# Kernel tuning notes

Measured on AMD Instinct MI355X. Metric: run time of the kernel, lower is better.

The kernel has to match this reference:

```python
import jax, jax.numpy as jnp
import numpy as np

H = 12          # heads in the ViT blocks
D = 768         # model dim (hard-coded in the module)
DFF = 3072      # mlp hidden = 4*D
ADIM = 64       # adapter bottleneck dim
L = 32          # num_latents
EPS = 1e-6      # timm ViT LayerNorm eps


def _ln(x, g, b):
    m = jnp.mean(x, axis=-1, keepdims=True)
    v = jnp.var(x, axis=-1, keepdims=True)
    return (x - m) * jax.lax.rsqrt(v + EPS) * g + b


def _quick_gelu(x):
    return x * jax.nn.sigmoid(1.702 * x)


def _sh_attn(q, k, v):
    # single-head attention used by fusion(); scale = C**-0.5 with C = full dim
    C = q.shape[-1]
    a = jax.nn.softmax(jnp.einsum('bnc,bmc->bnm', q, k) * (C ** -0.5), axis=-1)
    return jnp.einsum('bnm,bmc->bnc', a, v)


def _mhsa(x, qkv_w, qkv_b, proj_w, proj_b):
    B, N, C = x.shape
    Dh = C // H
    qkv = (x @ qkv_w.T + qkv_b).reshape(B, N, 3, H, Dh).transpose(2, 0, 3, 1, 4)
    q, k, v = qkv[0], qkv[1], qkv[2]                       # [B,H,N,Dh]
    a = jax.nn.softmax(jnp.einsum('bhnd,bhmd->bhnm', q, k) * (Dh ** -0.5), axis=-1)
    o = jnp.einsum('bhnm,bhmd->bhnd', a, v).transpose(0, 2, 1, 3).reshape(B, N, C)
    return o @ proj_w.T + proj_b


def _stream(t, ln1_g, ln1_b, qkv_w, qkv_b, proj_w, proj_b,
            ln2_g, ln2_b, fc1_w, fc1_b, fc2_w, fc2_b,
            down_w, down_b, up_w, up_b, scale):
    t = t + _mhsa(_ln(t, ln1_g, ln1_b), qkv_w, qkv_b, proj_w, proj_b)
    h = _ln(t, ln2_g, ln2_b)
    mlp = jax.nn.gelu(h @ fc1_w.T + fc1_b, approximate=False) @ fc2_w.T + fc2_b
    adapter = (_quick_gelu(h @ down_w.T + down_b) @ up_w.T + up_b) * scale
    return t + mlp + adapter


def setup_inputs() -> dict:
    key = jax.random.key(0)
    ks = iter(jax.random.split(key, 64))
    f32 = jnp.float32
    def rn(shape, std=0.02):
        return (jax.random.normal(next(ks), shape, dtype=f32) * std)
    inp = {
        'x': jax.random.normal(next(ks), (16, 512, 768), dtype=f32),
        'y': jax.random.normal(next(ks), (16, 196, 768), dtype=f32),
        'latents': rn((1, L, D)),
        'scale_a': jnp.full((1,), 0.5, f32),
        'scale_v': jnp.full((1,), 0.5, f32),
    }
    for p in ('spec', 'rgb'):
        inp.update({
            f'{p}_ln1_g': jnp.ones((D,), f32), f'{p}_ln1_b': jnp.zeros((D,), f32),
            f'{p}_qkv_w': rn((3 * D, D)), f'{p}_qkv_b': jnp.zeros((3 * D,), f32),
            f'{p}_proj_w': rn((D, D)), f'{p}_proj_b': jnp.zeros((D,), f32),
            f'{p}_ln2_g': jnp.ones((D,), f32), f'{p}_ln2_b': jnp.zeros((D,), f32),
            f'{p}_fc1_w': rn((DFF, D)), f'{p}_fc1_b': jnp.zeros((DFF,), f32),
            f'{p}_fc2_w': rn((D, DFF)), f'{p}_fc2_b': jnp.zeros((D,), f32),
            f'{p}_down_w': rn((ADIM, D)), f'{p}_down_b': jnp.zeros((ADIM,), f32),
            f'{p}_up_w': rn((D, ADIM)), f'{p}_up_b': jnp.zeros((D,), f32),
            f'{p}_scale': jnp.ones((1,), f32),
        })
    return inp


def reference(x, y, latents, scale_a, scale_v,
              spec_ln1_g, spec_ln1_b, spec_qkv_w, spec_qkv_b, spec_proj_w, spec_proj_b,
              spec_ln2_g, spec_ln2_b, spec_fc1_w, spec_fc1_b, spec_fc2_w, spec_fc2_b,
              spec_down_w, spec_down_b, spec_up_w, spec_up_b, spec_scale,
              rgb_ln1_g, rgb_ln1_b, rgb_qkv_w, rgb_qkv_b, rgb_proj_w, rgb_proj_b,
              rgb_ln2_g, rgb_ln2_b, rgb_fc1_w, rgb_fc1_b, rgb_fc2_w, rgb_fc2_b,
              rgb_down_w, rgb_down_b, rgb_up_w, rgb_up_b, rgb_scale):
    B = x.shape[0]
    # --- fusion via latent bottleneck (single-head attention) ---
    concat_ = jnp.concatenate((x, y), axis=1)                 # [B, Na+Nv, D]
    lat = jnp.broadcast_to(latents, (B, L, D))
    fused = _sh_attn(lat, concat_, concat_)                   # [B, L, D]
    x = x + scale_a * _sh_attn(x, fused, fused)
    y = y + scale_v * _sh_attn(y, fused, fused)
    # --- per-stream transformer block + adapter (dropout = eval/identity) ---
    x = _stream(x, spec_ln1_g, spec_ln1_b, spec_qkv_w, spec_qkv_b, spec_proj_w, spec_proj_b,
                spec_ln2_g, spec_ln2_b, spec_fc1_w, spec_fc1_b, spec_fc2_w, spec_fc2_b,
                spec_down_w, spec_down_b, spec_up_w, spec_up_b, spec_scale)
    y = _stream(y, rgb_ln1_g, rgb_ln1_b, rgb_qkv_w, rgb_qkv_b, rgb_proj_w, rgb_proj_b,
                rgb_ln2_g, rgb_ln2_b, rgb_fc1_w, rgb_fc1_b, rgb_fc2_w, rgb_fc2_b,
                rgb_down_w, rgb_down_b, rgb_up_w, rgb_up_b, rgb_scale)
    return (x, y)
```

## Files before the change

### kernel.cpp

```cpp
#include <hip/hip_runtime.h>
#include <hip/hip_bf16.h>


#define H_HEADS 12
#define DMODEL 768
#define DFF 3072
#define ADIM 64
#define NLAT 32
#define BATCH 16
#define NA 512
#define NV 196
#define NTOT 708
#define MCAT (BATCH * NTOT)
#define MTOT (BATCH * (NA + NV))

typedef __hip_bfloat16 bf16;
using bf16x8 = __attribute__((ext_vector_type(8))) short;
using f32x4  = __attribute__((ext_vector_type(4))) float;

static __device__ __forceinline__ float bf2f(bf16 v) { return __bfloat162float(v); }
static __device__ __forceinline__ float bflo(unsigned u) { return __uint_as_float(u << 16); }
static __device__ __forceinline__ float ld1(const float* p) { return *p; }
static __device__ __forceinline__ float ld1(const bf16* p) { return bf2f(*p); }
static __device__ __forceinline__ unsigned short f2bf_bits(float v) {
    unsigned u = __float_as_uint(v);
    return (unsigned short)((u + 0x7fffu + ((u >> 16) & 1u)) >> 16);
}

#define GLD_LDS16(gp, lp) __builtin_amdgcn_global_load_lds( \
    (const __attribute__((address_space(1))) void*)(gp), \
    (__attribute__((address_space(3))) void*)(lp), 16, 0, 0)

static inline int pad8(int v) { return (v + 7) & ~7; }

__global__ void detect_dtype_kernel(const unsigned short* __restrict__ x, int* __restrict__ flag)
{
    if (threadIdx.x == 0 && blockIdx.x == 0) {
        int big = 0;
        for (int i = 0; i < 2048; i++) {
            unsigned e = (x[i] >> 7) & 0xFF;
            if (e >= 0x90) big++;
        }
        flag[0] = (big > 16) ? 1 : 0;
        flag[1] = 0;
    }
}

template<typename TIn>
static __device__ __forceinline__ void pack_body(
    const TIn* __restrict__ x, const TIn* __restrict__ y, const TIn* __restrict__ lat,
    bf16* __restrict__ Cc, bf16* __restrict__ Lb)
{
    const int r = blockIdx.x, tid = threadIdx.x;
    const TIn* src;
    bf16* dst;
    if (r < MCAT) {
        const int b = r / NTOT, n = r - b * NTOT;
        src = (n < NA) ? x + ((size_t)(b * NA + n)) * DMODEL
                       : y + ((size_t)(b * NV + (n - NA))) * DMODEL;
        dst = Cc + (size_t)r * DMODEL;
    } else {
        src = lat + (size_t)(r - MCAT) * DMODEL;
        dst = Lb + (size_t)(r - MCAT) * DMODEL;
    }
    dst[tid]       = __float2bfloat16(ld1(src + tid));
    dst[tid + 256] = __float2bfloat16(ld1(src + tid + 256));
    dst[tid + 512] = __float2bfloat16(ld1(src + tid + 512));
}

__global__ __launch_bounds__(256)
void pack_concat_kernel(const int* __restrict__ flag, const void* x, const void* y,
                        const void* lat, bf16* __restrict__ Cc, bf16* __restrict__ Lb)
{
    if (flag[0]) pack_body<float>((const float*)x, (const float*)y, (const float*)lat, Cc, Lb);
    else         pack_body<bf16>((const bf16*)x, (const bf16*)y, (const bf16*)lat, Cc, Lb);
}

__global__ __launch_bounds__(64)
void fusion_softmax_kernel(const float* __restrict__ scores, float* __restrict__ P)
{
    const int b = blockIdx.x >> 5, l = blockIdx.x & 31, lane = threadIdx.x;
    const float* sp = scores + (size_t)b * NTOT * NLAT + l;
    float v[12];
    float mx = -1e30f;
    #pragma unroll
    for (int i = 0; i < 12; i++) {
        const int n = lane + i * 64;
        v[i] = (n < NTOT) ? sp[(size_t)n * NLAT] * 0.03608439182435161f : -1e30f;
        mx = fmaxf(mx, v[i]);
    }
    #pragma unroll
    for (int off = 32; off; off >>= 1) mx = fmaxf(mx, __shfl_xor(mx, off));
    float den = 0.f;
    #pragma unroll
    for (int i = 0; i < 12; i++) { v[i] = __expf(v[i] - mx); den += v[i]; }
    #pragma unroll
    for (int off = 32; off; off >>= 1) den += __shfl_xor(den, off);
    const float inv = 1.0f / den;
    float* op = P + ((size_t)b * NLAT + l) * 768;
    #pragma unroll
    for (int i = 0; i < 12; i++) {
        const int n = lane + i * 64;
        op[n] = (n < NTOT) ? v[i] * inv : 0.f;
    }
}

__global__ __launch_bounds__(256)
void fusion_wsum_kernel(const bf16* __restrict__ Cc, const float* __restrict__ P,
                        bf16* __restrict__ fused)
{
    const int b = blockIdx.y, d0 = blockIdx.x * 128;
    const int tid = threadIdx.x;
    const int lg = tid >> 5, dg = tid & 31;
    const int l0 = lg * 4;

    __shared__ float Ct[64][132];
    __shared__ float Ps[32][68];

    float acc[4][4] = {};

    for (int nc = 0; nc < 12; nc++) {
        const int n0 = nc * 64;
        __syncthreads();
        #pragma unroll
        for (int it = 0; it < 8; it++) {
            const int idx = it * 1024 + tid * 4;
            const int r = idx >> 7, c = idx & 127;
            const int gn = n0 + r;
            float4 v = make_float4(0.f, 0.f, 0.f, 0.f);
            if (gn < NTOT) {
                const ushort4 u = *(const ushort4*)(Cc + ((size_t)(b * NTOT + gn)) * DMODEL + d0 + c);
                v = make_float4(bflo(u.x), bflo(u.y), bflo(u.z), bflo(u.w));
            }
            Ct[r][c] = v.x; Ct[r][c + 1] = v.y; Ct[r][c + 2] = v.z; Ct[r][c + 3] = v.w;
        }
        {
            const int l = tid >> 3, off = (tid & 7) * 8;
            const float* pp = P + ((size_t)b * NLAT + l) * 768 + n0 + off;
            const float4 p0 = *(const float4*)pp;
            const float4 p1 = *(const float4*)(pp + 4);
            Ps[l][off] = p0.x; Ps[l][off + 1] = p0.y; Ps[l][off + 2] = p0.z; Ps[l][off + 3] = p0.w;
            Ps[l][off + 4] = p1.x; Ps[l][off + 5] = p1.y; Ps[l][off + 6] = p1.z; Ps[l][off + 7] = p1.w;
        }
        __syncthreads();

        for (int n = 0; n < 64; n++) {
            const float4 v = *(const float4*)&Ct[n][dg * 4];
            #pragma unroll
            for (int i = 0; i < 4; i++) {
                const float p = Ps[l0 + i][n];
                acc[i][0] += p * v.x; acc[i][1] += p * v.y;
                acc[i][2] += p * v.z; acc[i][3] += p * v.w;
            }
        }
    }

    #pragma unroll
    for (int i = 0; i < 4; i++) {
        bf16* op = fused + ((size_t)b * NLAT + l0 + i) * DMODEL + d0 + dg * 4;
        #pragma unroll
        for (int j = 0; j < 4; j++) op[j] = __float2bfloat16(acc[i][j]);
    }
}

template<typename TIn>
static __device__ __forceinline__ void attend_fused_body(
    const TIn* __restrict__ t, const bf16* __restrict__ fused,
    const TIn* __restrict__ scale_p, const TIn* __restrict__ lng, const TIn* __restrict__ lnb,
    bf16* __restrict__ out, bf16* __restrict__ hout, int Npb)
{
    const int tid = threadIdx.x;
    const int gid = blockIdx.x;
    const int b = gid / Npb;
    const TIn* row = t + (size_t)gid * DMODEL;
    const bf16* fb = fused + (size_t)b * NLAT * DMODEL;

    __shared__ float q[DMODEL];
    __shared__ float p[NLAT];
    __shared__ float rs[4], rq[4];

    for (int d = tid; d < DMODEL; d += 256) q[d] = ld1(row + d);
    __syncthreads();

    const int g = tid >> 3, li = tid & 7;
    float s = 0.f;
    const bf16* fr = fb + (size_t)g * DMODEL;
    for (int d = li; d < DMODEL; d += 8) s += q[d] * bf2f(fr[d]);
    s += __shfl_xor(s, 1); s += __shfl_xor(s, 2); s += __shfl_xor(s, 4);
    if (li == 0) p[g] = s * 0.03608439182435161f;
    __syncthreads();

    float mx = -1e30f;
    #pragma unroll
    for (int l = 0; l < NLAT; l++) mx = fmaxf(mx, p[l]);
    float w[NLAT];
    float den = 0.f;
    #pragma unroll
    for (int l = 0; l < NLAT; l++) { w[l] = __expf(p[l] - mx); den += w[l]; }
    const float sA = ld1(scale_p) / den;

    float a0 = 0.f, a1 = 0.f, a2 = 0.f;
    #pragma unroll
    for (int l = 0; l < NLAT; l++) {
        const bf16* fv = fb + (size_t)l * DMODEL;
        a0 += w[l] * bf2f(fv[tid]);
        a1 += w[l] * bf2f(fv[tid + 256]);
        a2 += w[l] * bf2f(fv[tid + 512]);
    }
    const float t0v = q[tid] + sA * a0;
    const float t1v = q[tid + 256] + sA * a1;
    const float t2v = q[tid + 512] + sA * a2;
    bf16* o = out + (size_t)gid * DMODEL;
    o[tid]       = __float2bfloat16(t0v);
    o[tid + 256] = __float2bfloat16(t1v);
    o[tid + 512] = __float2bfloat16(t2v);

    if (hout) {
        float ss = t0v + t1v + t2v;
        float sq = t0v * t0v + t1v * t1v + t2v * t2v;
        #pragma unroll
        for (int off = 32; off; off >>= 1) { ss += __shfl_xor(ss, off); sq += __shfl_xor(sq, off); }
        if ((tid & 63) == 0) { rs[tid >> 6] = ss; rq[tid >> 6] = sq; }
        __syncthreads();
        ss = rs[0] + rs[1] + rs[2] + rs[3];
        sq = rq[0] + rq[1] + rq[2] + rq[3];
        const float mean = ss * (1.0f / DMODEL);
        const float var = sq * (1.0f / DMODEL) - mean * mean;
        const float r = rsqrtf(var + 1e-6f);
        bf16* ho = hout + (size_t)gid * DMODEL;
        ho[tid]       = __float2bfloat16((t0v - mean) * r * ld1(lng + tid)       + ld1(lnb + tid));
        ho[tid + 256] = __float2bfloat16((t1v - mean) * r * ld1(lng + tid + 256) + ld1(lnb + tid + 256));
        ho[tid + 512] = __float2bfloat16((t2v - mean) * r * ld1(lng + tid + 512) + ld1(lnb + tid + 512));
    }
}

__global__ __launch_bounds__(256)
void attend_fused_kernel(const int* __restrict__ flag, const void* t, const bf16* __restrict__ fused,
                         const void* scale_p, const void* lng, const void* lnb,
                         bf16* __restrict__ out, bf16* __restrict__ hout, int Npb)
{
    if (flag[0]) attend_fused_body<float>((const float*)t, fused, (const float*)scale_p,
                                          (const float*)lng, (const float*)lnb, out, hout, Npb);
    else         attend_fused_body<bf16>((const bf16*)t, fused, (const bf16*)scale_p,
                                         (const bf16*)lng, (const bf16*)lnb, out, hout, Npb);
}

template<typename TW>
static __device__ __forceinline__ void ln_body(
    const bf16* __restrict__ in, const TW* __restrict__ g,
    const TW* __restrict__ bta, bf16* __restrict__ out)
{
    const int tid = threadIdx.x;
    const bf16* p = in + (size_t)blockIdx.x * DMODEL;
    const float v0 = bf2f(p[tid]), v1 = bf2f(p[tid + 256]), v2 = bf2f(p[tid + 512]);
    float s = v0 + v1 + v2;
    float sq = v0 * v0 + v1 * v1 + v2 * v2;
    #pragma unroll
    for (int off = 32; off; off >>= 1) { s += __shfl_xor(s, off); sq += __shfl_xor(sq, off); }
    __shared__ float rs[4], rq[4];
    if ((tid & 63) == 0) { rs[tid >> 6] = s; rq[tid >> 6] = sq; }
    __syncthreads();
    s = rs[0] + rs[1] + rs[2] + rs[3];
    sq = rq[0] + rq[1] + rq[2] + rq[3];
    const float mean = s * (1.0f / DMODEL);
    const float var = sq * (1.0f / DMODEL) - mean * mean;
    const float r = rsqrtf(var + 1e-6f);
    bf16* o = out + (size_t)blockIdx.x * DMODEL;
    o[tid]       = __float2bfloat16((v0 - mean) * r * ld1(g + tid)       + ld1(bta + tid));
    o[tid + 256] = __float2bfloat16((v1 - mean) * r * ld1(g + tid + 256) + ld1(bta + tid + 256));
    o[tid + 512] = __float2bfloat16((v2 - mean) * r * ld1(g + tid + 512) + ld1(bta + tid + 512));
}

__global__ __launch_bounds__(256)
void ln_kernel(const int* __restrict__ flag, const bf16* __restrict__ in,
               const void* g0, const void* b0, const void* g1, const void* b1,
               bf16* __restrict__ out, int split)
{
    const bool isY = (int)blockIdx.x >= split;
    const void* g = isY ? g1 : g0;
    const void* b = isY ? b1 : b0;
    if (flag[0]) ln_body<float>(in, (const float*)g, (const float*)b, out);
    else         ln_body<bf16>(in, (const bf16*)g, (const bf16*)b, out);
}

__global__ __launch_bounds__(256)
void flash_attn_kernel(const bf16* __restrict__ qkv, bf16* __restrict__ o, int Npb)
{
    const int tid = threadIdx.x;
    const int wv = tid >> 6, lane = tid & 63;
    const int l15 = lane & 15, q4 = lane >> 4;
    const int h = blockIdx.x % H_HEADS, bb = blockIdx.x / H_HEADS;
    const int qt = blockIdx.y;
    const int nkv = (Npb + 63) >> 6;
    const size_t tokbase = (size_t)bb * Npb;

    __shared__ __align__(16) short Ks[64 * 64];
    __shared__ __align__(16) short Vt[64 * 64];
    __shared__ __align__(16) short Ps[4][16 * 64];

    const int qr = min(qt * 64 + wv * 16 + l15, Npb - 1);
    const bf16* qp = qkv + (tokbase + qr) * 2304 + h * 64;
    const bf16x8 qf0 = *(const bf16x8*)(const void*)(qp + q4 * 8);
    const bf16x8 qf1 = *(const bf16x8*)(const void*)(qp + 32 + q4 * 8);

    f32x4 Oa[4] = {};
    float mrow[4], lrow[4];
    #pragma unroll
    for (int i = 0; i < 4; i++) { mrow[i] = -1e30f; lrow[i] = 0.f; }

    for (int kv = 0; kv < nkv; kv++) {
        const int kv0 = kv * 64;
        __syncthreads();
        #pragma unroll
        for (int inst = 0; inst < 2; inst++) {
            const int s = inst * 256 + tid;
            const int row = s >> 3, pos = s & 7;
            const int c = pos ^ (row & 7);
            const int krc = min(kv0 + row, Npb - 1);
            GLD_LDS16(qkv + (tokbase + krc) * 2304 + DMODEL + h * 64 + c * 8, &Ks[s * 8]);
        }
        {
            const int r = tid >> 2;
            const int f0 = (tid & 3) * 16;
            const int krc = min(kv0 + r, Npb - 1);
            const short* vp = (const short*)(qkv + (tokbase + krc) * 2304 + 2 * DMODEL + h * 64 + f0);
            short vb[16];
            *(uint4*)&vb[0] = *(const uint4*)vp;
            *(uint4*)&vb[8] = *(const uint4*)(vp + 8);
            const int chunk = r >> 3, r7 = r & 7;
            #pragma unroll
            for (int j = 0; j < 16; j++) {
                const int feat = f0 + j;
                Vt[feat * 64 + (chunk ^ (feat & 7)) * 8 + r7] = vb[j];
            }
        }
        __syncthreads();

        f32x4 s4[4] = {};
        #pragma unroll
        for (int kk = 0; kk < 2; kk++) {
            const bf16x8 qf = kk ? qf1 : qf0;
            const int c = kk * 4 + q4;
            #pragma unroll
            for (int g = 0; g < 4; g++) {
                const int r = g * 16 + l15;
                const bf16x8 kf = *(const bf16x8*)(const void*)&Ks[r * 64 + (c ^ (r & 7)) * 8];
                s4[g] = __builtin_amdgcn_mfma_f32_16x16x32_bf16(qf, kf, s4[g], 0, 0, 0);
            }
        }
        float tmax[4];
        #pragma unroll
        for (int i = 0; i < 4; i++) tmax[i] = -1e30f;
        #pragma unroll
        for (int g = 0; g < 4; g++) {
            const bool valid = (kv0 + g * 16 + l15) < Npb;
            #pragma unroll
            for (int i = 0; i < 4; i++) {
                const float v = s4[g][i] * 0.125f;
                s4[g][i] = valid ? v : -1e30f;
                tmax[i] = fmaxf(tmax[i], s4[g][i]);
            }
        }
        #pragma unroll
        for (int off = 1; off < 16; off <<= 1)
            #pragma unroll
            for (int i = 0; i < 4; i++) tmax[i] = fmaxf(tmax[i], __shfl_xor(tmax[i], off));
        float alpha[4], rsum[4];
        #pragma unroll
        for (int i = 0; i < 4; i++) {
            const float mn = fmaxf(mrow[i], tmax[i]);
            alpha[i] = __expf(mrow[i] - mn);
            mrow[i] = mn;
            rsum[i] = 0.f;
        }
        #pragma unroll
        for (int g = 0; g < 4; g++) {
            const int cc = g * 16 + l15;
            const int chunk = cc >> 3;
            #pragma unroll
            for (int i = 0; i < 4; i++) {
                const int r = q4 * 4 + i;
                const float p = __expf(s4[g][i] - mrow[i]);
                rsum[i] += p;
                Ps[wv][r * 64 + (chunk ^ (r & 7)) * 8 + (cc & 7)] = (short)f2bf_bits(p);
            }
        }
        #pragma unroll
        for (int off = 1; off < 16; off <<= 1)
            #pragma unroll
            for (int i = 0; i < 4; i++) rsum[i] += __shfl_xor(rsum[i], off);
        #pragma unroll
        for (int i = 0; i < 4; i++) lrow[i] = lrow[i] * alpha[i] + rsum[i];
        #pragma unroll
        for (int g = 0; g < 4; g++)
            #pragma unroll
            for (int i = 0; i < 4; i++) Oa[g][i] *= alpha[i];

        #pragma unroll
        for (int kk = 0; kk < 2; kk++) {
            const int c = kk * 4 + q4;
            const bf16x8 pf = *(const bf16x8*)(const void*)&Ps[wv][l15 * 64 + (c ^ (l15 & 7)) * 8];
            #pragma unroll
            for (int g = 0; g < 4; g++) {
                const int feat = g * 16 + l15;
                const bf16x8 vf = *(const bf16x8*)(const void*)&Vt[feat * 64 + (c ^ (feat & 7)) * 8];
                Oa[g] = __builtin_amdgcn_mfma_f32_16x16x32_bf16(pf, vf, Oa[g], 0, 0, 0);
            }
        }
    }

    float inv[4];
    #pragma unroll
    for (int i = 0; i < 4; i++) inv[i] = 1.0f / lrow[i];
    #pragma unroll
    for (int g = 0; g < 4; g++) {
        const int colo = h * 64 + g * 16 + l15;
        #pragma unroll
        for (int i = 0; i < 4; i++) {
            const int rowg = qt * 64 + wv * 16 + q4 * 4 + i;
            if (rowg < Npb)
                o[(tokbase + rowg) * DMODEL + colo] = __float2bfloat16(Oa[g][i] * inv[i]);
        }
    }
}

template<int TM, int ACT, bool RES, bool SCALE, bool FD, typename TW>
static __device__ __forceinline__ void gemm_body(
    const bf16* __restrict__ A, const TW* __restrict__ W, const TW* __restrict__ Wd,
    const TW* __restrict__ bias, const TW* __restrict__ biasd,
    const bf16* __restrict__ resid, const TW* __restrict__ scale_p,
    void* __restrict__ C, bf16* __restrict__ Cd,
    bool cf32, int row_off, int M, int N, int K,
    short* As, short* Bs, float* Ep)
{
    const int tid = threadIdx.x;
    const int lane = tid & 63;
    const int wv = tid >> 6;
    const int l15 = lane & 15, q4 = lane >> 4;
    const int m0 = blockIdx.x * TM, n0 = blockIdx.y * 128;
    const int N1 = FD ? N - ADIM : N;
    constexpr int NF = (TM == 128) ? 4 : 2;
    const int wm = (TM == 128) ? (wv & 1) * 64 : 0;
    const int wn = (TM == 128) ? (wv >> 1) * 64 : wv * 32;

    f32x4 acc[4][NF] = {};

    for (int k0 = 0; k0 < K; k0 += 64) {
        __syncthreads();
        constexpr int AIT = TM * 8 / 256;
        #pragma unroll
        for (int it = 0; it < AIT; it++) {
            const int i = it * 256 + tid;
            const int row = i >> 3, pos = i & 7;
            const int c = pos ^ (row & 7);
            const int ra = min(m0 + row, M - 1);
            GLD_LDS16(A + (size_t)ra * K + k0 + c * 8, &As[i * 8]);
        }
        #pragma unroll
        for (int it = 0; it < 4; it++) {
            const int i = it * 256 + tid;
            const int row = i >> 3, pos = i & 7;
            const int c = pos ^ (row & 7);
            const int rb = min(n0 + row, N - 1);
            const TW* wp = (FD && rb >= N1) ? Wd + (size_t)(rb - N1) * K : W + (size_t)rb * K;
            if constexpr (sizeof(TW) == 2) {
                GLD_LDS16(wp + k0 + c * 8, &Bs[i * 8]);
            } else {
                const float* fp = (const float*)wp + k0 + c * 8;
                const float4 w0 = *(const float4*)fp;
                const float4 w1 = *(const float4*)(fp + 4);
                unsigned short hb[8];
                hb[0] = f2bf_bits(w0.x); hb[1] = f2bf_bits(w0.y);
                hb[2] = f2bf_bits(w0.z); hb[3] = f2bf_bits(w0.w);
                hb[4] = f2bf_bits(w1.x); hb[5] = f2bf_bits(w1.y);
                hb[6] = f2bf_bits(w1.z); hb[7] = f2bf_bits(w1.w);
                *(uint4*)&Bs[i * 8] = *(const uint4*)hb;
            }
        }
        __syncthreads();

        #pragma unroll
        for (int kk = 0; kk < 2; kk++) {
            bf16x8 af[4], bfr[NF];
            #pragma unroll
            for (int f = 0; f < 4; f++) {
                const int r = wm + f * 16 + l15;
                af[f] = *(const bf16x8*)(const void*)&As[(r * 8 + ((kk * 4 + q4) ^ (r & 7))) * 8];
            }
            #pragma unroll
            for (int g = 0; g < NF; g++) {
                const int rn = wn + g * 16 + l15;
                bfr[g] = *(const bf16x8*)(const void*)&Bs[(rn * 8 + ((kk * 4 + q4) ^ (rn & 7))) * 8];
            }
            #pragma unroll
            for (int f = 0; f < 4; f++)
                #pragma unroll
                for (int g = 0; g < NF; g++)
                    acc[f][g] = __builtin_amdgcn_mfma_f32_16x16x32_bf16(af[f], bfr[g], acc[f][g], 0, 0, 0);
        }
    }
    __syncthreads();

    const float sc = SCALE ? ld1(scale_p) : 1.0f;
    constexpr int NPASS = (TM == 128) ? 2 : 1;
    #pragma unroll
    for (int pass = 0; pass < NPASS; pass++) {
        if (wm == pass * 64) {
            #pragma unroll
            for (int g = 0; g < NF; g++) {
                const int col = wn + g * 16 + l15;
                const int colg = n0 + col;
                const bool isdown = FD && (colg >= N1);
                const float bv = bias ? (isdown ? ld1(biasd + (colg - N1)) : ld1(bias + colg)) : 0.f;
                #pragma unroll
                for (int f = 0; f < 4; f++) {
                    #pragma unroll
                    for (int i = 0; i < 4; i++) {
                        const int row = f * 16 + q4 * 4 + i;
                        float v = acc[f][g][i] + bv;
                        if (FD) {
                            if (isdown) v = v / (1.0f + __expf(-1.702f * v));
                            else v = 0.5f * v * (1.0f + erff(v * 0.70710678118654752f));
                        } else if (ACT == 1) v = 0.5f * v * (1.0f + erff(v * 0.70710678118654752f));
                        else if (ACT == 2) v = v / (1.0f + __expf(-1.702f * v));
                        if (SCALE) v *= sc;
                        const int c = col >> 2;
                        Ep[row * 128 + (((c ^ (row & 31))) << 2) + (col & 3)] = v;
                    }
                }
            }
        }
        __syncthreads();
        #pragma unroll
        for (int it = 0; it < 8; it++) {
            const int cid = it * 256 + tid;
            const int row = cid >> 5, c = cid & 31;
            const int rowg = m0 + pass * 64 + row;
            const int colg = n0 + c * 4;
            if (rowg < M && colg < N) {
                f32x4 v = *(const f32x4*)&Ep[row * 128 + (((c ^ (row & 31))) << 2)];
                if (FD && colg >= N1) {
                    ushort4 u;
                    u.x = f2bf_bits(v[0]); u.y = f2bf_bits(v[1]);
                    u.z = f2bf_bits(v[2]); u.w = f2bf_bits(v[3]);
                    *(ushort4*)(Cd + (size_t)rowg * ADIM + (colg - N1)) = u;
                } else {
                    if (RES) {
                        const ushort4 r4 = *(const ushort4*)(resid + (size_t)rowg * N + colg);
                        v[0] += bflo(r4.x); v[1] += bflo(r4.y);
                        v[2] += bflo(r4.z); v[3] += bflo(r4.w);
                    }
                    if (cf32) {
                        *(f32x4*)((float*)C + (size_t)(rowg + row_off) * N + colg) = v;
                    } else {
                        ushort4 u;
                        u.x = f2bf_bits(v[0]); u.y = f2bf_bits(v[1]);
                        u.z = f2bf_bits(v[2]); u.w = f2bf_bits(v[3]);
                        *(ushort4*)((bf16*)C + (size_t)(rowg + row_off) * (FD ? N1 : N) + colg) = u;
                    }
                }
            }
        }
        if (pass + 1 < NPASS) __syncthreads();
    }
}

template<int TM, int ACT, bool RES, bool SCALE, bool FD>
__global__ __launch_bounds__(256)
void mfma_gemm_kernel(const int* __restrict__ flag, const bf16* __restrict__ A,
                      const void* W0, const void* W1, const void* Wd0, const void* Wd1,
                      const void* b0, const void* b1, const void* bd0, const void* bd1,
                      const bf16* __restrict__ resid, const void* sp0, const void* sp1,
                      void* __restrict__ C, bf16* __restrict__ Cd,
                      int out_mode, int row_off, int M, int N, int K, int split)
{
    __shared__ __align__(16) char SMEM[32768];
    if ((int)blockIdx.x * TM >= M) return;
    const bool isY = ((int)blockIdx.x * TM) >= split;
    const void* W = isY ? W1 : W0;
    const void* Wd = isY ? Wd1 : Wd0;
    const void* bb = isY ? b1 : b0;
    const void* bd = isY ? bd1 : bd0;
    const void* sp = isY ? sp1 : sp0;
    short* As = (short*)SMEM;
    short* Bs = As + TM * 64;
    float* Ep = (float*)SMEM;
    const bool cf32 = (out_mode == 2) || (out_mode == 1 && flag[0] != 0);
    if (flag[0])
        gemm_body<TM, ACT, RES, SCALE, FD, float>(A, (const float*)W, (const float*)Wd,
            (const float*)bb, (const float*)bd, resid, (const float*)sp, C, Cd,
            cf32, row_off, M, N, K, As, Bs, Ep);
    else
        gemm_body<TM, ACT, RES, SCALE, FD, bf16>(A, (const bf16*)W, (const bf16*)Wd,
            (const bf16*)bb, (const bf16*)bd, resid, (const bf16*)sp, C, Cd,
            cf32, row_off, M, N, K, As, Bs, Ep);
}

struct SW {
    const void *ln1_g, *ln1_b, *qkv_w, *qkv_b, *proj_w, *proj_b,
               *ln2_g, *ln2_b, *fc1_w, *fc1_b, *fc2_w, *fc2_b,
               *down_w, *down_b, *up_w, *up_b, *scale;
};

static void stream_seq(const int* flag, bf16* t0, bf16* h, bf16* big, bf16* ah,
                       int M, int split, const SW& a, const SW& b,
                       void* outC, int row_off,
                       int npb0, int rows0, int npb1, int rows1, hipStream_t s)
{
    const dim3 gq(pad8((M + 127) / 128), 18);
    const dim3 gf(pad8((M + 127) / 128), 25);
    const dim3 g7(pad8((M + 63) / 64), 6);

    mfma_gemm_kernel<128, 0, false, false, false><<<gq, 256, 0, s>>>(flag, h,
        a.qkv_w, b.qkv_w, nullptr, nullptr, a.qkv_b, b.qkv_b, nullptr, nullptr,
        nullptr, nullptr, nullptr, big, nullptr, 0, 0, M, 2304, DMODEL, split);
    flash_attn_kernel<<<dim3((rows0 / npb0) * H_HEADS, (npb0 + 63) / 64), 256, 0, s>>>(big, h, npb0);
    if (rows1)
        flash_attn_kernel<<<dim3((rows1 / npb1) * H_HEADS, (npb1 + 63) / 64), 256, 0, s>>>(
            big + (size_t)rows0 * 2304, h + (size_t)rows0 * DMODEL, npb1);
    mfma_gemm_kernel<64, 0, true, false, false><<<g7, 256, 0, s>>>(flag, h,
        a.proj_w, b.proj_w, nullptr, nullptr, a.proj_b, b.proj_b, nullptr, nullptr,
        t0, nullptr, nullptr, t0, nullptr, 0, 0, M, DMODEL, DMODEL, split);
    ln_kernel<<<M, 256, 0, s>>>(flag, t0, a.ln2_g, a.ln2_b, b.ln2_g, b.ln2_b, h, split);
    mfma_gemm_kernel<128, 1, false, false, true><<<gf, 256, 0, s>>>(flag, h,
        a.fc1_w, b.fc1_w, a.down_w, b.down_w, a.fc1_b, b.fc1_b, a.down_b, b.down_b,
        nullptr, nullptr, nullptr, big, ah, 0, 0, M, DFF + ADIM, DMODEL, split);
    mfma_gemm_kernel<64, 0, true, false, false><<<g7, 256, 0, s>>>(flag, big,
        a.fc2_w, b.fc2_w, nullptr, nullptr, a.fc2_b, b.fc2_b, nullptr, nullptr,
        t0, nullptr, nullptr, t0, nullptr, 0, 0, M, DMODEL, DFF, split);
    mfma_gemm_kernel<64, 0, true, true, false><<<g7, 256, 0, s>>>(flag, ah,
        a.up_w, b.up_w, nullptr, nullptr, a.up_b, b.up_b, nullptr, nullptr,
        t0, a.scale, b.scale, outC, nullptr, 1, row_off, M, DMODEL, ADIM, split);
}

extern "C" void kernel_launch(void* const* d_in, const int* in_sizes, int n_in,
                              void* d_out, int out_size, void* d_ws, size_t ws_size,
                              hipStream_t stream)
{
    SW sw, rw;
    auto fill = [&](SW& s, int base) {
        s.ln1_g = d_in[base + 0];  s.ln1_b = d_in[base + 1];
        s.qkv_w = d_in[base + 2];  s.qkv_b = d_in[base + 3];
        s.proj_w = d_in[base + 4]; s.proj_b = d_in[base + 5];
        s.ln2_g = d_in[base + 6];  s.ln2_b = d_in[base + 7];
        s.fc1_w = d_in[base + 8];  s.fc1_b = d_in[base + 9];
        s.fc2_w = d_in[base + 10]; s.fc2_b = d_in[base + 11];
        s.down_w = d_in[base + 12]; s.down_b = d_in[base + 13];
        s.up_w = d_in[base + 14];  s.up_b = d_in[base + 15];
        s.scale = d_in[base + 16];
    };
    fill(sw, 5);
    fill(rw, 22);

    const int Mx = BATCH * NA;
    const int My = BATCH * NV;
    const int NOSPLIT = 1 << 30;

    const size_t szA = 256 + ((size_t)MTOT * DMODEL * 2 + (size_t)BATCH * NLAT * DMODEL
                     + (size_t)MTOT * DFF + (size_t)MTOT * ADIM) * 2;
    const size_t szB = 256 + ((size_t)Mx * DMODEL * 2 + (size_t)My * DMODEL
                     + (size_t)BATCH * NLAT * DMODEL + (size_t)Mx * DFF + (size_t)Mx * ADIM) * 2;

    int* flag = (int*)d_ws;
    detect_dtype_kernel<<<1, 64, 0, stream>>>((const unsigned short*)d_in[0], flag);

    if (ws_size >= szA) {
        char* base = (char*)d_ws + 256;
        bf16* t0 = (bf16*)base;      base += (size_t)MTOT * DMODEL * 2;
        bf16* fused = (bf16*)base;   base += (size_t)BATCH * NLAT * DMODEL * 2;
        bf16* h = (bf16*)base;       base += (size_t)MTOT * DMODEL * 2;
        bf16* big = (bf16*)base;     base += (size_t)MTOT * DFF * 2;
        bf16* ah = (bf16*)base;

        bf16* Cc = h;
        bf16* Lb = ah;
        float* scores = (float*)big;
        float* P = (float*)((char*)big + 2 * 1024 * 1024);

        pack_concat_kernel<<<MCAT + NLAT, 256, 0, stream>>>(flag, d_in[0], d_in[1], d_in[2], Cc, Lb);
        mfma_gemm_kernel<128, 0, false, false, false><<<dim3(pad8((MCAT + 127) / 128), 1), 256, 0, stream>>>(
            flag + 1, Cc, Lb, Lb, nullptr, nullptr, nullptr, nullptr, nullptr, nullptr,
            nullptr, nullptr, nullptr, scores, nullptr, 2, 0, MCAT, NLAT, DMODEL, NOSPLIT);
        fusion_softmax_kernel<<<BATCH * NLAT, 64, 0, stream>>>(scores, P);
        fusion_wsum_kernel<<<dim3(DMODEL / 128, BATCH), 256, 0, stream>>>(Cc, P, fused);

        attend_fused_kernel<<<BATCH * NA, 256, 0, stream>>>(
            flag, d_in[0], fused, d_in[3], sw.ln1_g, sw.ln1_b, t0, h, NA);
        attend_fused_kernel<<<BATCH * NV, 256, 0, stream>>>(
            flag, d_in[1], fused, d_in[4], rw.ln1_g, rw.ln1_b,
            t0 + (size_t)Mx * DMODEL, h + (size_t)Mx * DMODEL, NV);

        stream_seq(flag, t0, h, big, ah, MTOT, Mx, sw, rw, d_out, 0,
                   NA, Mx, NV, My, stream);
    } else if (ws_size >= szB) {
        char* base = (char*)d_ws + 256;
        bf16* x1 = (bf16*)base;      base += (size_t)Mx * DMODEL * 2;
        bf16* y1 = (bf16*)base;      base += (size_t)My * DMODEL * 2;
        bf16* fused = (bf16*)base;   base += (size_t)BATCH * NLAT * DMODEL * 2;
        bf16* h = (bf16*)base;       base += (size_t)Mx * DMODEL * 2;
        bf16* big = (bf16*)base;     base += (size_t)Mx * DFF * 2;
        bf16* ah = (bf16*)base;

        bf16* Cc = big;
        bf16* Lb = ah;
        float* scores = (float*)((char*)big + 18 * 1024 * 1024);
        float* P = (float*)((char*)big + 20 * 1024 * 1024);

        pack_concat_kernel<<<MCAT + NLAT, 256, 0, stream>>>(flag, d_in[0], d_in[1], d_in[2], Cc, Lb);
        mfma_gemm_kernel<128, 0, false, false, false><<<dim3(pad8((MCAT + 127) / 128), 1), 256, 0, stream>>>(
            flag + 1, Cc, Lb, Lb, nullptr, nullptr, nullptr, nullptr, nullptr, nullptr,
            nullptr, nullptr, nullptr, scores, nullptr, 2, 0, MCAT, NLAT, DMODEL, NOSPLIT);
        fusion_softmax_kernel<<<BATCH * NLAT, 64, 0, stream>>>(scores, P);
        fusion_wsum_kernel<<<dim3(DMODEL / 128, BATCH), 256, 0, stream>>>(Cc, P, fused);

        attend_fused_kernel<<<BATCH * NA, 256, 0, stream>>>(
            flag, d_in[0], fused, d_in[3], sw.ln1_g, sw.ln1_b, x1, h, NA);
        stream_seq(flag, x1, h, big, ah, Mx, NOSPLIT, sw, sw, d_out, 0, NA, Mx, 0, 0, stream);

        attend_fused_kernel<<<BATCH * NV, 256, 0, stream>>>(
            flag, d_in[1], fused, d_in[4], rw.ln1_g, rw.ln1_b, y1, h, NV);
        stream_seq(flag, y1, h, big, ah, My, NOSPLIT, rw, rw, d_out, Mx, NV, My, 0, 0, stream);
    } else {
        char* base = (char*)d_ws + 256;
        bf16* x1 = (bf16*)base;      base += (size_t)Mx * DMODEL * 2;
        bf16* y1 = (bf16*)base;      base += (size_t)My * DMODEL * 2;
        bf16* fused = (bf16*)base;   base += (size_t)BATCH * NLAT * DMODEL * 2;
        bf16* h = (bf16*)base;       base += (size_t)My * DMODEL * 2;
        bf16* big = (bf16*)base;     base += (size_t)My * DFF * 2;
        bf16* ah = (bf16*)base;

        bf16* Cc = big;
        bf16* Lb = ah;
        float* scores = (float*)((char*)big + 17500160);
        float* P = (float*)h;

        pack_concat_kernel<<<MCAT + NLAT, 256, 0, stream>>>(flag, d_in[0], d_in[1], d_in[2], Cc, Lb);
        mfma_gemm_kernel<128, 0, false, false, false><<<dim3(pad8((MCAT + 127) / 128), 1), 256, 0, stream>>>(
            flag + 1, Cc, Lb, Lb, nullptr, nullptr, nullptr, nullptr, nullptr, nullptr,
            nullptr, nullptr, nullptr, scores, nullptr, 2, 0, MCAT, NLAT, DMODEL, NOSPLIT);
        fusion_softmax_kernel<<<BATCH * NLAT, 64, 0, stream>>>(scores, P);
        fusion_wsum_kernel<<<dim3(DMODEL / 128, BATCH), 256, 0, stream>>>(Cc, P, fused);

        attend_fused_kernel<<<BATCH * NA, 256, 0, stream>>>(
            flag, d_in[0], fused, d_in[3], sw.ln1_g, sw.ln1_b, x1, nullptr, NA);
        const int MCH = 2048;
        for (int c = 0; c < Mx / MCH; c++) {
            bf16* t0c = x1 + (size_t)c * MCH * DMODEL;
            ln_kernel<<<MCH, 256, 0, stream>>>(flag, t0c, sw.ln1_g, sw.ln1_b,
                                               sw.ln1_g, sw.ln1_b, h, NOSPLIT);
            stream_seq(flag, t0c, h, big, ah, MCH, NOSPLIT, sw, sw, d_out, c * MCH,
                       NA, MCH, 0, 0, stream);
        }
        attend_fused_kernel<<<BATCH * NV, 256, 0, stream>>>(
            flag, d_in[1], fused, d_in[4], rw.ln1_g, rw.ln1_b, y1, h, NV);
        stream_seq(flag, y1, h, big, ah, My, NOSPLIT, rw, rw, d_out, Mx, NV, My, 0, 0, stream);
    }
}
```

Measured before the change: 1.205 ms.

## Use uniform 128x128 GEMM tiles with BK=32 and XCD-aware 1D block mapping

Replaces the two GEMM tile variants (128x128 and 64x128, BK=64) with a single 128x128 tile using a 32-wide K step and half the shared memory. Block indices are remapped onto a 1D grid so consecutive M tiles land on the same XCD while N tiles vary, aiming for better L2 reuse of A rows. Smaller LDS use may allow more resident blocks per CU. The costs are twice as many K iterations and barriers, and the 768-wide GEMMs now run with fewer, larger blocks.

```diff
diff --git a/kernel.cpp b/kernel.cpp
--- a/kernel.cpp
+++ b/kernel.cpp
@@ -30,8 +30,6 @@
 #define GLD_LDS16(gp, lp) __builtin_amdgcn_global_load_lds( \
     (const __attribute__((address_space(1))) void*)(gp), \
     (__attribute__((address_space(3))) void*)(lp), 16, 0, 0)
-
-static inline int pad8(int v) { return (v + 7) & ~7; }
 
 __global__ void detect_dtype_kernel(const unsigned short* __restrict__ x, int* __restrict__ flag)
 {
@@ -424,47 +422,37 @@
     }
 }
 
-template<int TM, int ACT, bool RES, bool SCALE, bool FD, typename TW>
+template<int ACT, bool RES, bool SCALE, bool FD, typename TW>
 static __device__ __forceinline__ void gemm_body(
     const bf16* __restrict__ A, const TW* __restrict__ W, const TW* __restrict__ Wd,
     const TW* __restrict__ bias, const TW* __restrict__ biasd,
     const bf16* __restrict__ resid, const TW* __restrict__ scale_p,
     void* __restrict__ C, bf16* __restrict__ Cd,
-    bool cf32, int row_off, int M, int N, int K,
+    bool cf32, int row_off, int m0, int n0, int M, int N, int K,
     short* As, short* Bs, float* Ep)
 {
     const int tid = threadIdx.x;
     const int lane = tid & 63;
     const int wv = tid >> 6;
     const int l15 = lane & 15, q4 = lane >> 4;
-    const int m0 = blockIdx.x * TM, n0 = blockIdx.y * 128;
     const int N1 = FD ? N - ADIM : N;
-    constexpr int NF = (TM == 128) ? 4 : 2;
-    const int wm = (TM == 128) ? (wv & 1) * 64 : 0;
-    const int wn = (TM == 128) ? (wv >> 1) * 64 : wv * 32;
-
-    f32x4 acc[4][NF] = {};
-
-    for (int k0 = 0; k0 < K; k0 += 64) {
+    const int wm = (wv & 1) * 64, wn = (wv >> 1) * 64;
+
+    f32x4 acc[4][4] = {};
+
+    for (int k0 = 0; k0 < K; k0 += 32) {
         __syncthreads();
-        constexpr int AIT = TM * 8 / 256;
-        #pragma unroll
-        for (int it = 0; it < AIT; it++) {
-            const int i = it * 256 + tid;
-            const int row = i >> 3, pos = i & 7;
-            const int c = pos ^ (row & 7);
+        #pragma unroll
+        for (int inst = 0; inst < 2; inst++) {
+            const int s = inst * 256 + tid;
+            const int row = s >> 2, pos = s & 3;
+            const int c = pos ^ ((row >> 1) & 3);
             const int ra = min(m0 + row, M - 1);
-            GLD_LDS16(A + (size_t)ra * K + k0 + c * 8, &As[i * 8]);
-        }
-        #pragma unroll
-        for (int it = 0; it < 4; it++) {
-            const int i = it * 256 + tid;
-            const int row = i >> 3, pos = i & 7;
-            const int c = pos ^ (row & 7);
             const int rb = min(n0 + row, N - 1);
+            GLD_LDS16(A + (size_t)ra * K + k0 + c * 8, &As[s * 8]);
             const TW* wp = (FD && rb >= N1) ? Wd + (size_t)(rb - N1) * K : W + (size_t)rb * K;
             if constexpr (sizeof(TW) == 2) {
-                GLD_LDS16(wp + k0 + c * 8, &Bs[i * 8]);
+                GLD_LDS16(wp + k0 + c * 8, &Bs[s * 8]);
             } else {
                 const float* fp = (const float*)wp + k0 + c * 8;
                 const float4 w0 = *(const float4*)fp;
@@ -474,49 +462,43 @@
                 hb[2] = f2bf_bits(w0.z); hb[3] = f2bf_bits(w0.w);
                 hb[4] = f2bf_bits(w1.x); hb[5] = f2bf_bits(w1.y);
                 hb[6] = f2bf_bits(w1.z); hb[7] = f2bf_bits(w1.w);
-                *(uint4*)&Bs[i * 8] = *(const uint4*)hb;
+                *(uint4*)&Bs[s * 8] = *(const uint4*)hb;
             }
         }
         __syncthreads();
 
-        #pragma unroll
-        for (int kk = 0; kk < 2; kk++) {
-            bf16x8 af[4], bfr[NF];
-            #pragma unroll
-            for (int f = 0; f < 4; f++) {
-                const int r = wm + f * 16 + l15;
-                af[f] = *(const bf16x8*)(const void*)&As[(r * 8 + ((kk * 4 + q4) ^ (r & 7))) * 8];
-            }
-            #pragma unroll
-            for (int g = 0; g < NF; g++) {
-                const int rn = wn + g * 16 + l15;
-                bfr[g] = *(const bf16x8*)(const void*)&Bs[(rn * 8 + ((kk * 4 + q4) ^ (rn & 7))) * 8];
-            }
-            #pragma unroll
-            for (int f = 0; f < 4; f++)
-                #pragma unroll
-                for (int g = 0; g < NF; g++)
-                    acc[f][g] = __builtin_amdgcn_mfma_f32_16x16x32_bf16(af[f], bfr[g], acc[f][g], 0, 0, 0);
-        }
+        bf16x8 af[4], bfr[4];
+        #pragma unroll
+        for (int f = 0; f < 4; f++) {
+            const int r = wm + f * 16 + l15;
+            af[f] = *(const bf16x8*)(const void*)&As[r * 32 + (q4 ^ ((r >> 1) & 3)) * 8];
+            const int rn = wn + f * 16 + l15;
+            bfr[f] = *(const bf16x8*)(const void*)&Bs[rn * 32 + (q4 ^ ((rn >> 1) & 3)) * 8];
+        }
+        #pragma unroll
+        for (int f = 0; f < 4; f++)
+            #pragma unroll
+            for (int g = 0; g < 4; g++)
+                acc[f][g] = __builtin_amdgcn_mfma_f32_16x16x32_bf16(af[f], bfr[g], acc[f][g], 0, 0, 0);
     }
     __syncthreads();
 
     const float sc = SCALE ? ld1(scale_p) : 1.0f;
-    constexpr int NPASS = (TM == 128) ? 2 : 1;
-    #pragma unroll
-    for (int pass = 0; pass < NPASS; pass++) {
-        if (wm == pass * 64) {
-            #pragma unroll
-            for (int g = 0; g < NF; g++) {
-                const int col = wn + g * 16 + l15;
-                const int colg = n0 + col;
+    #pragma unroll
+    for (int p = 0; p < 4; p++) {
+        const int rh = p >> 1, ch = p & 1;
+        if (wm == rh * 64 && wn == ch * 64) {
+            #pragma unroll
+            for (int g = 0; g < 4; g++) {
+                const int col_loc = g * 16 + l15;
+                const int colg = n0 + ch * 64 + col_loc;
                 const bool isdown = FD && (colg >= N1);
                 const float bv = bias ? (isdown ? ld1(biasd + (colg - N1)) : ld1(bias + colg)) : 0.f;
                 #pragma unroll
                 for (int f = 0; f < 4; f++) {
                     #pragma unroll
                     for (int i = 0; i < 4; i++) {
-                        const int row = f * 16 + q4 * 4 + i;
+                        const int row_loc = f * 16 + q4 * 4 + i;
                         float v = acc[f][g][i] + bv;
                         if (FD) {
                             if (isdown) v = v / (1.0f + __expf(-1.702f * v));
@@ -524,21 +506,21 @@
                         } else if (ACT == 1) v = 0.5f * v * (1.0f + erff(v * 0.70710678118654752f));
                         else if (ACT == 2) v = v / (1.0f + __expf(-1.702f * v));
                         if (SCALE) v *= sc;
-                        const int c = col >> 2;
-                        Ep[row * 128 + (((c ^ (row & 31))) << 2) + (col & 3)] = v;
+                        const int c4 = col_loc >> 2;
+                        Ep[row_loc * 64 + ((c4 ^ (row_loc & 15)) << 2) + (col_loc & 3)] = v;
                     }
                 }
             }
         }
         __syncthreads();
         #pragma unroll
-        for (int it = 0; it < 8; it++) {
-            const int cid = it * 256 + tid;
-            const int row = cid >> 5, c = cid & 31;
-            const int rowg = m0 + pass * 64 + row;
-            const int colg = n0 + c * 4;
+        for (int it = 0; it < 4; it++) {
+            const int row = it * 16 + (tid >> 4);
+            const int c4 = tid & 15;
+            const int rowg = m0 + rh * 64 + row;
+            const int colg = n0 + ch * 64 + c4 * 4;
             if (rowg < M && colg < N) {
-                f32x4 v = *(const f32x4*)&Ep[row * 128 + (((c ^ (row & 31))) << 2)];
+                f32x4 v = *(const f32x4*)&Ep[row * 64 + ((c4 ^ (row & 15)) << 2)];
                 if (FD && colg >= N1) {
                     ushort4 u;
                     u.x = f2bf_bits(v[0]); u.y = f2bf_bits(v[1]);
@@ -561,11 +543,11 @@
                 }
             }
         }
-        if (pass + 1 < NPASS) __syncthreads();
-    }
-}
-
-template<int TM, int ACT, bool RES, bool SCALE, bool FD>
+        if (p < 3) __syncthreads();
+    }
+}
+
+template<int ACT, bool RES, bool SCALE, bool FD>
 __global__ __launch_bounds__(256)
 void mfma_gemm_kernel(const int* __restrict__ flag, const bf16* __restrict__ A,
                       const void* W0, const void* W1, const void* Wd0, const void* Wd1,
@@ -574,26 +556,39 @@
                       void* __restrict__ C, bf16* __restrict__ Cd,
                       int out_mode, int row_off, int M, int N, int K, int split)
 {
-    __shared__ __align__(16) char SMEM[32768];
-    if ((int)blockIdx.x * TM >= M) return;
-    const bool isY = ((int)blockIdx.x * TM) >= split;
+    __shared__ __align__(16) char SMEM[16384];
+    const int NT = (N + 127) >> 7;
+    const int MT = (M + 127) >> 7;
+    const int xcd = blockIdx.x & 7;
+    const int idx = blockIdx.x >> 3;
+    const int n_t = idx % NT;
+    const int m_t = (idx / NT) * 8 + xcd;
+    if (m_t >= MT) return;
+    const int m0 = m_t << 7, n0 = n_t << 7;
+
+    const bool isY = m0 >= split;
     const void* W = isY ? W1 : W0;
     const void* Wd = isY ? Wd1 : Wd0;
     const void* bb = isY ? b1 : b0;
     const void* bd = isY ? bd1 : bd0;
     const void* sp = isY ? sp1 : sp0;
     short* As = (short*)SMEM;
-    short* Bs = As + TM * 64;
+    short* Bs = As + 128 * 32;
     float* Ep = (float*)SMEM;
     const bool cf32 = (out_mode == 2) || (out_mode == 1 && flag[0] != 0);
     if (flag[0])
-        gemm_body<TM, ACT, RES, SCALE, FD, float>(A, (const float*)W, (const float*)Wd,
+        gemm_body<ACT, RES, SCALE, FD, float>(A, (const float*)W, (const float*)Wd,
             (const float*)bb, (const float*)bd, resid, (const float*)sp, C, Cd,
-            cf32, row_off, M, N, K, As, Bs, Ep);
+            cf32, row_off, m0, n0, M, N, K, As, Bs, Ep);
     else
-        gemm_body<TM, ACT, RES, SCALE, FD, bf16>(A, (const bf16*)W, (const bf16*)Wd,
+        gemm_body<ACT, RES, SCALE, FD, bf16>(A, (const bf16*)W, (const bf16*)Wd,
             (const bf16*)bb, (const bf16*)bd, resid, (const bf16*)sp, C, Cd,
-            cf32, row_off, M, N, K, As, Bs, Ep);
+            cf32, row_off, m0, n0, M, N, K, As, Bs, Ep);
+}
+
+static inline int gemm_grid(int M, int N) {
+    const int MT = (M + 127) / 128, NT = (N + 127) / 128;
+    return 8 * ((MT + 7) / 8) * NT;
 }
 
 struct SW {
@@ -607,28 +602,24 @@
                        void* outC, int row_off,
                        int npb0, int rows0, int npb1, int rows1, hipStream_t s)
 {
-    const dim3 gq(pad8((M + 127) / 128), 18);
-    const dim3 gf(pad8((M + 127) / 128), 25);
-    const dim3 g7(pad8((M + 63) / 64), 6);
-
-    mfma_gemm_kernel<128, 0, false, false, false><<<gq, 256, 0, s>>>(flag, h,
+    mfma_gemm_kernel<0, false, false, false><<<gemm_grid(M, 2304), 256, 0, s>>>(flag, h,
         a.qkv_w, b.qkv_w, nullptr, nullptr, a.qkv_b, b.qkv_b, nullptr, nullptr,
         nullptr, nullptr, nullptr, big, nullptr, 0, 0, M, 2304, DMODEL, split);
     flash_attn_kernel<<<dim3((rows0 / npb0) * H_HEADS, (npb0 + 63) / 64), 256, 0, s>>>(big, h, npb0);
     if (rows1)
         flash_attn_kernel<<<dim3((rows1 / npb1) * H_HEADS, (npb1 + 63) / 64), 256, 0, s>>>(
             big + (size_t)rows0 * 2304, h + (size_t)rows0 * DMODEL, npb1);
-    mfma_gemm_kernel<64, 0, true, false, false><<<g7, 256, 0, s>>>(flag, h,
+    mfma_gemm_kernel<0, true, false, false><<<gemm_grid(M, DMODEL), 256, 0, s>>>(flag, h,
         a.proj_w, b.proj_w, nullptr, nullptr, a.proj_b, b.proj_b, nullptr, nullptr,
         t0, nullptr, nullptr, t0, nullptr, 0, 0, M, DMODEL, DMODEL, split);
     ln_kernel<<<M, 256, 0, s>>>(flag, t0, a.ln2_g, a.ln2_b, b.ln2_g, b.ln2_b, h, split);
-    mfma_gemm_kernel<128, 1, false, false, true><<<gf, 256, 0, s>>>(flag, h,
+    mfma_gemm_kernel<1, false, false, true><<<gemm_grid(M, DFF + ADIM), 256, 0, s>>>(flag, h,
         a.fc1_w, b.fc1_w, a.down_w, b.down_w, a.fc1_b, b.fc1_b, a.down_b, b.down_b,
         nullptr, nullptr, nullptr, big, ah, 0, 0, M, DFF + ADIM, DMODEL, split);
-    mfma_gemm_kernel<64, 0, true, false, false><<<g7, 256, 0, s>>>(flag, big,
+    mfma_gemm_kernel<0, true, false, false><<<gemm_grid(M, DMODEL), 256, 0, s>>>(flag, big,
         a.fc2_w, b.fc2_w, nullptr, nullptr, a.fc2_b, b.fc2_b, nullptr, nullptr,
         t0, nullptr, nullptr, t0, nullptr, 0, 0, M, DMODEL, DFF, split);
-    mfma_gemm_kernel<64, 0, true, true, false><<<g7, 256, 0, s>>>(flag, ah,
+    mfma_gemm_kernel<0, true, true, false><<<gemm_grid(M, DMODEL), 256, 0, s>>>(flag, ah,
         a.up_w, b.up_w, nullptr, nullptr, a.up_b, b.up_b, nullptr, nullptr,
         t0, a.scale, b.scale, outC, nullptr, 1, row_off, M, DMODEL, ADIM, split);
 }
@@ -678,7 +669,7 @@
         float* P = (float*)((char*)big + 2 * 1024 * 1024);
 
         pack_concat_kernel<<<MCAT + NLAT, 256, 0, stream>>>(flag, d_in[0], d_in[1], d_in[2], Cc, Lb);
-        mfma_gemm_kernel<128, 0, false, false, false><<<dim3(pad8((MCAT + 127) / 128), 1), 256, 0, stream>>>(
+        mfma_gemm_kernel<0, false, false, false><<<gemm_grid(MCAT, NLAT), 256, 0, stream>>>(
             flag + 1, Cc, Lb, Lb, nullptr, nullptr, nullptr, nullptr, nullptr, nullptr,
             nullptr, nullptr, nullptr, scores, nullptr, 2, 0, MCAT, NLAT, DMODEL, NOSPLIT);
         fusion_softmax_kernel<<<BATCH * NLAT, 64, 0, stream>>>(scores, P);
@@ -707,7 +698,7 @@
         float* P = (float*)((char*)big + 20 * 1024 * 1024);
 
         pack_concat_kernel<<<MCAT + NLAT, 256, 0, stream>>>(flag, d_in[0], d_in[1], d_in[2], Cc, Lb);
-        mfma_gemm_kernel<128, 0, false, false, false><<<dim3(pad8((MCAT + 127) / 128), 1), 256, 0, stream>>>(
+        mfma_gemm_kernel<0, false, false, false><<<gemm_grid(MCAT, NLAT), 256, 0, stream>>>(
             flag + 1, Cc, Lb, Lb, nullptr, nullptr, nullptr, nullptr, nullptr, nullptr,
             nullptr, nullptr, nullptr, scores, nullptr, 2, 0, MCAT, NLAT, DMODEL, NOSPLIT);
         fusion_softmax_kernel<<<BATCH * NLAT, 64, 0, stream>>>(scores, P);
@@ -735,7 +726,7 @@
         float* P = (float*)h;
 
         pack_concat_kernel<<<MCAT + NLAT, 256, 0, stream>>>(flag, d_in[0], d_in[1], d_in[2], Cc, Lb);
-        mfma_gemm_kernel<128, 0, false, false, false><<<dim3(pad8((MCAT + 127) / 128), 1), 256, 0, stream>>>(
+        mfma_gemm_kernel<0, false, false, false><<<gemm_grid(MCAT, NLAT), 256, 0, stream>>>(
             flag + 1, Cc, Lb, Lb, nullptr, nullptr, nullptr, nullptr, nullptr, nullptr,
             nullptr, nullptr, nullptr, scores, nullptr, 2, 0, MCAT, NLAT, DMODEL, NOSPLIT);
         fusion_softmax_kernel<<<BATCH * NLAT, 64, 0, stream>>>(scores, P);
```

Measured after the change: 1.367 ms. +13.4%, slower.
